# Kernel tuning notes

Measured on AMD Instinct MI355X. Metric: run time of the kernel, lower is better.

## Reference

```python
import jax, jax.numpy as jnp
import numpy as np

N_ENT, N_REL = 100000, 500
D1, D2 = 200, 200
OC, FW = 32, 9            # out_channels, filt_w (filt_h = 1, in_channels = 1)
B = 4096
W_IN = 2 * D1             # 400 = concat(e1, e2)
W_OUT = W_IN - FW + 1     # 392
FC_LEN = OC * W_OUT       # 12544
FC1_LEN = OC * FW         # 288
EPS = 1e-5


def setup_inputs() -> dict:
    key = jax.random.key(0)
    ks = jax.random.split(key, 8)
    return {
        "e1_idx": jax.random.randint(ks[0], (B,), 0, N_ENT),
        "r_idx": jax.random.randint(ks[1], (B,), 0, N_REL),
        "e2_idx": jax.random.randint(ks[2], (B,), 0, N_ENT),
        "E_table": jax.random.normal(ks[3], (N_ENT, D1), jnp.float32) * 0.1,
        "R_table": jax.random.normal(ks[4], (N_REL, D2), jnp.float32) * 0.1,
        "bn0_gamma": jnp.ones((1,), jnp.float32),
        "bn0_beta": jnp.zeros((1,), jnp.float32),
        "bn0_mean": jnp.zeros((1,), jnp.float32),
        "bn0_var": jnp.ones((1,), jnp.float32),
        "fc1_w": jax.random.normal(ks[5], (FC1_LEN, D2), jnp.float32) * 0.05,
        "fc1_b": jnp.zeros((FC1_LEN,), jnp.float32),
        "bn1_gamma": jnp.ones((OC,), jnp.float32),
        "bn1_beta": jnp.zeros((OC,), jnp.float32),
        "bn1_mean": jnp.zeros((OC,), jnp.float32),
        "bn1_var": jnp.ones((OC,), jnp.float32),
        "fc_w": jax.random.normal(ks[6], (W_IN, FC_LEN), jnp.float32) * 0.02,
        "fc_b": jnp.zeros((W_IN,), jnp.float32),
        "bn2_gamma": jnp.ones((W_IN,), jnp.float32),
        "bn2_beta": jnp.zeros((W_IN,), jnp.float32),
        "bn2_mean": jnp.zeros((W_IN,), jnp.float32),
        "bn2_var": jnp.ones((W_IN,), jnp.float32),
        "fc2_w": jax.random.normal(ks[7], (1, W_IN), jnp.float32) * 0.05,
        "fc2_b": jnp.zeros((1,), jnp.float32),
        "bias": jnp.zeros((1,), jnp.float32),
    }


def reference(e1_idx, r_idx, e2_idx, E_table, R_table,
              bn0_gamma, bn0_beta, bn0_mean, bn0_var,
              fc1_w, fc1_b,
              bn1_gamma, bn1_beta, bn1_mean, bn1_var,
              fc_w, fc_b,
              bn2_gamma, bn2_beta, bn2_mean, bn2_var,
              fc2_w, fc2_b, bias):
    # Embedding lookups; E = concat(e1, e2) along feature dim -> [B, 400]
    e1 = E_table[e1_idx]
    e2 = E_table[e2_idx]
    E = jnp.concatenate([e1, e2], axis=-1)

    # bn0 over the single input channel (eval-mode batchnorm)
    x = (E - bn0_mean[0]) * (bn0_gamma[0] / jnp.sqrt(bn0_var[0] + EPS)) + bn0_beta[0]

    # Hypernetwork: per-example conv filters [B, OC, FW]
    r = R_table[r_idx]
    k = (r @ fc1_w.T + fc1_b).reshape(-1, OC, FW)

    # Grouped (per-example) 1x9 convolution, valid padding.
    # Sliding windows: [B, W_OUT, FW] (loop over FW=9 taps only)
    xw = jnp.stack([x[:, j:j + W_OUT] for j in range(FW)], axis=-1)
    conv = jnp.einsum('bwj,boj->bow', xw, k)  # [B, OC, W_OUT]

    # bn1 over OC channels (eval mode)
    inv1 = bn1_gamma / jnp.sqrt(bn1_var + EPS)
    y = (conv - bn1_mean[None, :, None]) * inv1[None, :, None] + bn1_beta[None, :, None]

    # flatten in [B, OC, 1, W_OUT] contiguous order -> [B, OC*W_OUT]
    flat = y.reshape(y.shape[0], -1)

    h = flat @ fc_w.T + fc_b                                   # [B, 400]
    h = (h - bn2_mean) * (bn2_gamma / jnp.sqrt(bn2_var + EPS)) + bn2_beta
    out = jnp.tanh(h @ fc2_w.T + fc2_b) + bias                 # [B, 1]
    return out
```

## Files before the change

kernel.cpp:

```cpp
#include <hip/hip_runtime.h>

#define BATCH   4096
#define N_REL   500
#define D1      200
#define W_IN    400
#define OC      32
#define FW      9
#define W_OUT   392
#define FC_LEN  12544
#define FC1_LEN 288
#define EPS     1e-5f

#define OSPLIT  8
#define OCH     50
#define WBLK    49
#define CHUNK   512


__global__ __launch_bounds__(256)
void ab_k(const float* __restrict__ R, const float* __restrict__ fc1w,
          const float* __restrict__ fc1b,
          const float* __restrict__ g1, const float* __restrict__ v1,
          const float* __restrict__ fcw, const float* __restrict__ g2,
          const float* __restrict__ v2, const float* __restrict__ fc2w,
          float* __restrict__ KR, float* __restrict__ wpart)
{
    __shared__ float sm[D1];
    const int bx = blockIdx.x;
    const int t  = threadIdx.x;

    if (bx < N_REL) {
        if (t < D1) sm[t] = R[(size_t)bx * D1 + t];
        __syncthreads();
        for (int i = t; i < FC1_LEN; i += 256) {
            const float4* wrow = (const float4*)(fc1w + (size_t)i * D1);
            float acc = fc1b[i];
            #pragma unroll 10
            for (int c = 0; c < D1 / 4; ++c) {
                float4 wv = wrow[c];
                acc += sm[c * 4 + 0] * wv.x + sm[c * 4 + 1] * wv.y
                     + sm[c * 4 + 2] * wv.z + sm[c * 4 + 3] * wv.w;
            }
            const int oc = i / FW;
            KR[(size_t)bx * FC1_LEN + i] = acc * (g1[oc] * rsqrtf(v1[oc] + EPS));
        }
    } else {
        const int v = bx - N_REL;
        const int y = v / WBLK, kb = v - y * WBLK;
        const int o0 = y * OCH;
        if (t < OCH) {
            const int o = o0 + t;
            sm[t] = fc2w[o] * g2[o] * rsqrtf(v2[o] + EPS);
        }
        __syncthreads();
        const int k = kb * 256 + t;
        float acc = 0.f;
        #pragma unroll 10
        for (int i = 0; i < OCH; ++i)
            acc += fcw[(size_t)(o0 + i) * FC_LEN + k] * sm[i];
        wpart[y * FC_LEN + k] = acc;
    }
}

__global__ __launch_bounds__(256)
void wsum_k(const float* __restrict__ wpart,
            const float* __restrict__ g1, const float* __restrict__ b1,
            const float* __restrict__ m1, const float* __restrict__ v1,
            const float* __restrict__ g2, const float* __restrict__ b2,
            const float* __restrict__ m2, const float* __restrict__ v2,
            const float* __restrict__ fcb, const float* __restrict__ fc2w,
            const float* __restrict__ fc2b,
            float* __restrict__ wbig, float* __restrict__ c3part)
{
    __shared__ float red[256];
    const int t = threadIdx.x;
    const int k = blockIdx.x * 256 + t;
    float w8 = 0.f;
    #pragma unroll
    for (int y = 0; y < OSPLIT; ++y) w8 += wpart[y * FC_LEN + k];
    wbig[k] = w8;
    const int oc = k / W_OUT;
    const float inv1 = g1[oc] * rsqrtf(v1[oc] + EPS);
    float pc = (b1[oc] - m1[oc] * inv1) * w8;
    if (blockIdx.x == 0) {
        for (int o = t; o < W_IN; o += 256) {
            const float s2 = g2[o] * rsqrtf(v2[o] + EPS);
            pc += (b2[o] - m2[o] * s2 + fcb[o] * s2) * fc2w[o];
        }
        if (t == 0) pc += fc2b[0];
    }
    red[t] = pc;
    __syncthreads();
    #pragma unroll
    for (int s = 128; s > 0; s >>= 1) {
        if (t < s) red[t] += red[t + s];
        __syncthreads();
    }
    if (t == 0) c3part[blockIdx.x] = red[0];
}

__global__ __launch_bounds__(256)
void prelfin_k(const int* __restrict__ e1i, const int* __restrict__ ri,
               const int* __restrict__ e2i, const float* __restrict__ E,
               const float* __restrict__ KR, const float* __restrict__ wbig,
               const float* __restrict__ c3part,
               const float* __restrict__ g0, const float* __restrict__ b0,
               const float* __restrict__ m0p, const float* __restrict__ v0,
               const float* __restrict__ bias,
               float* __restrict__ out)
{
    __shared__ __align__(16) float wls[FC_LEN];
    __shared__ float kfs[FC1_LEN];
    __shared__ float red[256];
    __shared__ float prow[W_IN];
    __shared__ float crelS;
    __shared__ int   list[CHUNK];
    __shared__ int   cnt;

    const int rel = blockIdx.x;
    const int t = threadIdx.x;
    const int wave = t >> 6, lane = t & 63;

    for (int i = t; i < FC_LEN / 4; i += 256)
        *(float4*)(wls + i * 4) = *(const float4*)(wbig + i * 4);
    for (int i = t; i < FC1_LEN; i += 256)
        kfs[i] = KR[(size_t)rel * FC1_LEN + i];
    __syncthreads();

    const float s0 = g0[0] * rsqrtf(v0[0] + EPS);
    const float t0 = b0[0] - m0p[0] * s0;

    float lsum = 0.f;
    for (int d = t; d < W_IN; d += 256) {
        const int jlo = (d > W_OUT - 1) ? d - (W_OUT - 1) : 0;
        const int jhi = (d < FW - 1) ? d : (FW - 1);
        float pp = 0.f;
        for (int oc = 0; oc < OC; ++oc) {
            const float* wb = wls + oc * W_OUT + d;
            const float* kk = kfs + oc * FW;
            for (int j = jlo; j <= jhi; ++j)
                pp += kk[j] * wb[-j];
        }
        lsum += pp;
        prow[d] = s0 * pp;
    }
    red[t] = lsum;
    __syncthreads();
    #pragma unroll
    for (int s = 128; s > 0; s >>= 1) {
        if (t < s) red[t] += red[t + s];
        __syncthreads();
    }
    if (t == 0) {
        float cgs = 0.f;
        for (int i = 0; i < WBLK; ++i) cgs += c3part[i];
        crelS = t0 * red[0] + cgs;
    }
    __syncthreads();

    const float cr = crelS;
    const float bi = bias[0];

    for (int c0 = 0; c0 < BATCH; c0 += CHUNK) {
        if (t == 0) cnt = 0;
        __syncthreads();
        for (int e = c0 + t; e < c0 + CHUNK; e += 256)
            if (ri[e] == rel) {
                const int idx = atomicAdd(&cnt, 1);
                list[idx] = e;
            }
        __syncthreads();
        const int n = cnt;
        for (int q = wave; q < n; q += 4) {
            const int e = list[q];
            const float* E1 = E + (size_t)e1i[e] * D1;
            const float* E2 = E + (size_t)e2i[e] * D1;
            float acc = 0.f;
            for (int d = lane; d < D1; d += 64) acc += E1[d] * prow[d];
            for (int d = lane; d < D1; d += 64) acc += E2[d] * prow[D1 + d];
            #pragma unroll
            for (int off = 32; off > 0; off >>= 1) acc += __shfl_down(acc, off);
            if (lane == 0) out[e] = tanhf(acc + cr) + bi;
        }
        __syncthreads();
    }
}

extern "C" void kernel_launch(void* const* d_in, const int* in_sizes, int n_in,
                              void* d_out, int out_size, void* d_ws, size_t ws_size,
                              hipStream_t stream)
{
    const int*   e1i  = (const int*)d_in[0];
    const int*   ri   = (const int*)d_in[1];
    const int*   e2i  = (const int*)d_in[2];
    const float* E    = (const float*)d_in[3];
    const float* R    = (const float*)d_in[4];
    const float* g0   = (const float*)d_in[5];
    const float* b0   = (const float*)d_in[6];
    const float* m0p  = (const float*)d_in[7];
    const float* v0   = (const float*)d_in[8];
    const float* fc1w = (const float*)d_in[9];
    const float* fc1b = (const float*)d_in[10];
    const float* g1   = (const float*)d_in[11];
    const float* b1   = (const float*)d_in[12];
    const float* m1   = (const float*)d_in[13];
    const float* v1   = (const float*)d_in[14];
    const float* fcw  = (const float*)d_in[15];
    const float* fcb  = (const float*)d_in[16];
    const float* g2   = (const float*)d_in[17];
    const float* b2   = (const float*)d_in[18];
    const float* m2   = (const float*)d_in[19];
    const float* v2   = (const float*)d_in[20];
    const float* fc2w = (const float*)d_in[21];
    const float* fc2b = (const float*)d_in[22];
    const float* bias = (const float*)d_in[23];

    char* ws = (char*)d_ws;
    float* KR     = (float*)(ws + 0);
    float* wpart  = (float*)(ws + 576000);
    float* wbig   = (float*)(ws + 977408);
    float* c3part = (float*)(ws + 1027584);
    (void)ws_size; (void)in_sizes; (void)n_in; (void)out_size;

    ab_k<<<N_REL + OSPLIT * WBLK, 256, 0, stream>>>(R, fc1w, fc1b, g1, v1,
                                                    fcw, g2, v2, fc2w, KR, wpart);
    wsum_k<<<WBLK, 256, 0, stream>>>(wpart, g1, b1, m1, v1, g2, b2, m2, v2,
                                     fcb, fc2w, fc2b, wbig, c3part);
    prelfin_k<<<N_REL, 256, 0, stream>>>(e1i, ri, e2i, E, KR, wbig, c3part,
                                         g0, b0, m0p, v0, bias, (float*)d_out);
}
```

Measured before the change: 237.0 us.

## Split per-relation prep from per-example dot and register-tile the transposed conv

The fused per-relation kernel, where each block scanned all 4096 relation indices in chunks to find its examples, is split in two. One kernel computes the per-relation projection vector P and its constant into workspace. A second kernel launches one wave per example and gathers P by relation index. The projection is now computed with zero-padded shared tiles, each of 100 threads producing 4 outputs from float4 loads and an unrolled 9-tap loop, which removes the divergent jlo/jhi bounds. This adds one kernel launch and an 800KB workspace round trip, but removes the serial chunk scan and atomic list building.

```diff
diff --git a/kernel.cpp b/kernel.cpp
--- a/kernel.cpp
+++ b/kernel.cpp
@@ -14,7 +14,7 @@
 #define OSPLIT  8
 #define OCH     50
 #define WBLK    49
-#define CHUNK   512
+#define WPADL   408
 
 
 __global__ __launch_bounds__(256)
@@ -100,49 +100,67 @@
 }
 
 __global__ __launch_bounds__(256)
-void prelfin_k(const int* __restrict__ e1i, const int* __restrict__ ri,
-               const int* __restrict__ e2i, const float* __restrict__ E,
-               const float* __restrict__ KR, const float* __restrict__ wbig,
-               const float* __restrict__ c3part,
-               const float* __restrict__ g0, const float* __restrict__ b0,
-               const float* __restrict__ m0p, const float* __restrict__ v0,
-               const float* __restrict__ bias,
-               float* __restrict__ out)
-{
-    __shared__ __align__(16) float wls[FC_LEN];
-    __shared__ float kfs[FC1_LEN];
+void prel_k(const float* __restrict__ KR, const float* __restrict__ wbig,
+            const float* __restrict__ c3part,
+            const float* __restrict__ g0, const float* __restrict__ b0,
+            const float* __restrict__ m0p, const float* __restrict__ v0,
+            float* __restrict__ Ps, float* __restrict__ crel)
+{
+    __shared__ __align__(16) float wpad[OC * WPADL];
+    __shared__ __align__(16) float kfp[OC * 12];
     __shared__ float red[256];
-    __shared__ float prow[W_IN];
-    __shared__ float crelS;
-    __shared__ int   list[CHUNK];
-    __shared__ int   cnt;
-
     const int rel = blockIdx.x;
     const int t = threadIdx.x;
-    const int wave = t >> 6, lane = t & 63;
-
-    for (int i = t; i < FC_LEN / 4; i += 256)
-        *(float4*)(wls + i * 4) = *(const float4*)(wbig + i * 4);
-    for (int i = t; i < FC1_LEN; i += 256)
-        kfs[i] = KR[(size_t)rel * FC1_LEN + i];
+
+    for (int u = t; u < OC * 16; u += 256) {
+        const int oc = u >> 4, x = u & 15;
+        wpad[oc * WPADL + (x < 8 ? x : 392 + x)] = 0.f;
+    }
+    for (int u = t; u < OC * 98; u += 256) {
+        const int oc = u / 98, c = u - oc * 98;
+        *(float4*)(wpad + oc * WPADL + 8 + c * 4) =
+            *(const float4*)(wbig + oc * W_OUT + c * 4);
+    }
+    for (int u = t; u < OC * 12; u += 256) {
+        const int oc = u / 12, j = u - oc * 12;
+        kfp[u] = (j < FW) ? KR[(size_t)rel * FC1_LEN + oc * FW + j] : 0.f;
+    }
     __syncthreads();
 
     const float s0 = g0[0] * rsqrtf(v0[0] + EPS);
     const float t0 = b0[0] - m0p[0] * s0;
 
     float lsum = 0.f;
-    for (int d = t; d < W_IN; d += 256) {
-        const int jlo = (d > W_OUT - 1) ? d - (W_OUT - 1) : 0;
-        const int jhi = (d < FW - 1) ? d : (FW - 1);
-        float pp = 0.f;
+    if (t < 100) {
+        const int d0 = t * 4;
+        float a0 = 0.f, a1 = 0.f, a2 = 0.f, a3 = 0.f;
         for (int oc = 0; oc < OC; ++oc) {
-            const float* wb = wls + oc * W_OUT + d;
-            const float* kk = kfs + oc * FW;
-            for (int j = jlo; j <= jhi; ++j)
-                pp += kk[j] * wb[-j];
-        }
-        lsum += pp;
-        prow[d] = s0 * pp;
+            const float* wb = wpad + oc * WPADL + d0;
+            float4 wA = *(const float4*)(wb);
+            float4 wB = *(const float4*)(wb + 4);
+            float4 wC = *(const float4*)(wb + 8);
+            const float w[12] = {wA.x, wA.y, wA.z, wA.w,
+                                 wB.x, wB.y, wB.z, wB.w,
+                                 wC.x, wC.y, wC.z, wC.w};
+            const float* kp = kfp + oc * 12;
+            float4 k0 = *(const float4*)(kp);
+            float4 k1 = *(const float4*)(kp + 4);
+            float4 k2 = *(const float4*)(kp + 8);
+            const float k[12] = {k0.x, k0.y, k0.z, k0.w,
+                                 k1.x, k1.y, k1.z, k1.w,
+                                 k2.x, k2.y, k2.z, k2.w};
+            #pragma unroll
+            for (int j = 0; j < FW; ++j) {
+                const float kj = k[j];
+                a0 += kj * w[8 - j];
+                a1 += kj * w[9 - j];
+                a2 += kj * w[10 - j];
+                a3 += kj * w[11 - j];
+            }
+        }
+        lsum = a0 + a1 + a2 + a3;
+        float4 o = {s0 * a0, s0 * a1, s0 * a2, s0 * a3};
+        *(float4*)(Ps + (size_t)rel * W_IN + d0) = o;
     }
     red[t] = lsum;
     __syncthreads();
@@ -154,36 +172,29 @@
     if (t == 0) {
         float cgs = 0.f;
         for (int i = 0; i < WBLK; ++i) cgs += c3part[i];
-        crelS = t0 * red[0] + cgs;
-    }
-    __syncthreads();
-
-    const float cr = crelS;
-    const float bi = bias[0];
-
-    for (int c0 = 0; c0 < BATCH; c0 += CHUNK) {
-        if (t == 0) cnt = 0;
-        __syncthreads();
-        for (int e = c0 + t; e < c0 + CHUNK; e += 256)
-            if (ri[e] == rel) {
-                const int idx = atomicAdd(&cnt, 1);
-                list[idx] = e;
-            }
-        __syncthreads();
-        const int n = cnt;
-        for (int q = wave; q < n; q += 4) {
-            const int e = list[q];
-            const float* E1 = E + (size_t)e1i[e] * D1;
-            const float* E2 = E + (size_t)e2i[e] * D1;
-            float acc = 0.f;
-            for (int d = lane; d < D1; d += 64) acc += E1[d] * prow[d];
-            for (int d = lane; d < D1; d += 64) acc += E2[d] * prow[D1 + d];
-            #pragma unroll
-            for (int off = 32; off > 0; off >>= 1) acc += __shfl_down(acc, off);
-            if (lane == 0) out[e] = tanhf(acc + cr) + bi;
-        }
-        __syncthreads();
-    }
+        crel[rel] = t0 * red[0] + cgs;
+    }
+}
+
+__global__ __launch_bounds__(256)
+void final_k(const int* __restrict__ e1i, const int* __restrict__ ri,
+             const int* __restrict__ e2i,
+             const float* __restrict__ E, const float* __restrict__ Ps,
+             const float* __restrict__ crel, const float* __restrict__ bias,
+             float* __restrict__ out)
+{
+    const int wave = threadIdx.x >> 6, lane = threadIdx.x & 63;
+    const int e = blockIdx.x * 4 + wave;
+    const int i1 = e1i[e], i2 = e2i[e], rel = ri[e];
+    const float* P  = Ps + (size_t)rel * W_IN;
+    const float* E1 = E + (size_t)i1 * D1;
+    const float* E2 = E + (size_t)i2 * D1;
+    float acc = 0.f;
+    for (int d = lane; d < D1; d += 64) acc += E1[d] * P[d];
+    for (int d = lane; d < D1; d += 64) acc += E2[d] * P[D1 + d];
+    #pragma unroll
+    for (int off = 32; off > 0; off >>= 1) acc += __shfl_down(acc, off);
+    if (lane == 0) out[e] = tanhf(acc + crel[rel]) + bias[0];
 }
 
 extern "C" void kernel_launch(void* const* d_in, const int* in_sizes, int n_in,
@@ -220,12 +231,15 @@
     float* wpart  = (float*)(ws + 576000);
     float* wbig   = (float*)(ws + 977408);
     float* c3part = (float*)(ws + 1027584);
+    float* Ps     = (float*)(ws + 1027840);
+    float* crel   = (float*)(ws + 1827840);
     (void)ws_size; (void)in_sizes; (void)n_in; (void)out_size;
 
     ab_k<<<N_REL + OSPLIT * WBLK, 256, 0, stream>>>(R, fc1w, fc1b, g1, v1,
                                                     fcw, g2, v2, fc2w, KR, wpart);
     wsum_k<<<WBLK, 256, 0, stream>>>(wpart, g1, b1, m1, v1, g2, b2, m2, v2,
                                      fcb, fc2w, fc2b, wbig, c3part);
-    prelfin_k<<<N_REL, 256, 0, stream>>>(e1i, ri, e2i, E, KR, wbig, c3part,
-                                         g0, b0, m0p, v0, bias, (float*)d_out);
-}
+    prel_k<<<N_REL, 256, 0, stream>>>(KR, wbig, c3part, g0, b0, m0p, v0, Ps, crel);
+    final_k<<<BATCH / 4, 256, 0, stream>>>(e1i, ri, e2i, E, Ps, crel, bias,
+                                           (float*)d_out);
+}
```

Measured after the change: 192.6 us. -18.8%, faster.
